# Performance work log

Measured on AMD Instinct MI355X. Metric: run time of the kernel, lower is better.

The kernel has to match this reference:

```python
import jax, jax.numpy as jnp
import numpy as np

B, EMB, ARRAY = 4096, 512, 2
KW = KH = KC = 8
OC = 16                      # output_channel per branch
RED = OC * 2                 # SE hidden width
NUM_REL = 500
FC_IN = 3 * OC * KH * KW * KC  # 24576, flattened concat of 3 branches


def _make_chequer_perm():
    # Deterministic replication of MSLE.get_chequer_perm (perm=1).
    rng = np.random.RandomState(0)
    ent_perm = rng.permutation(EMB * (ARRAY - 1))
    rel_perm = rng.permutation(EMB)
    idxs, ei, ri = [], 0, 0
    for i in range(KC):
        for j in range(KH):
            for k in range(KW):
                for m in range(ARRAY):
                    if (i + j) % ARRAY == m:
                        idxs.append(int(rel_perm[ri]) + EMB * (ARRAY - 1)); ri += 1
                    else:
                        idxs.append(int(ent_perm[ei])); ei += 1
    return jnp.asarray(np.asarray(idxs, dtype=np.int32))


def setup_inputs() -> dict:
    key = jax.random.key(0)
    ks = jax.random.split(key, 12)
    n = lambda k, shape, s=0.05: jax.random.normal(k, shape, jnp.float32) * s
    f1_dim = ARRAY * OC * 1 * 1 * ARRAY        # (1,1,2) kernels
    f3_dim = ARRAY * OC * 1 * ARRAY * ARRAY    # (1,2,2) kernels
    f5_dim = ARRAY * OC * ARRAY * ARRAY * ARRAY  # (2,2,2) kernels
    z = lambda shape: jnp.zeros(shape, jnp.float32)
    o = lambda shape: jnp.ones(shape, jnp.float32)
    return {
        "concat_input": jax.random.normal(ks[0], (B, EMB * ARRAY), jnp.float32),
        "rel": jax.random.randint(ks[1], (B,), 0, NUM_REL),
        "chequer_perm": _make_chequer_perm(),
        "f1_table": n(ks[2], (NUM_REL, f1_dim)),
        "f3_table": n(ks[3], (NUM_REL, f3_dim)),
        "f5_table": n(ks[4], (NUM_REL, f5_dim)),
        "bn0_g": o((ARRAY,)), "bn0_b": z((ARRAY,)),
        "bn1_g": o((OC,)), "bn1_b": z((OC,)),
        "bn2_g": o((OC,)), "bn2_b": z((OC,)),
        "bn3_g": o((OC,)), "bn3_b": z((OC,)),
        "att_Wsq": n(ks[5], (OC, RED)), "att_bsq": z((RED,)),
        "att_W1": n(ks[6], (RED, OC)), "att_b1": z((OC,)),
        "att_W2": n(ks[7], (RED, OC)), "att_b2": z((OC,)),
        "att_W3": n(ks[8], (RED, OC)), "att_b3": z((OC,)),
        "fc_W": n(ks[9], (FC_IN, EMB), 0.01), "fc_b": z((EMB,)),
    }


def _bn(x, g, b, eps=1e-5):
    # BatchNorm3d, training-mode batch statistics over (N, D, H, W).
    m = x.mean(axis=(0, 2, 3, 4), keepdims=True)
    v = x.var(axis=(0, 2, 3, 4), keepdims=True)
    sh = (1, -1, 1, 1, 1)
    return (x - m) * jax.lax.rsqrt(v + eps) * g.reshape(sh) + b.reshape(sh)


def _per_sample_conv(x, w):
    # x: (B, Cin, D, H, W); w: (B, Cout, Cin, kd, kh, kw). 'same' padding,
    # even kernels pad the extra element at the high end (torch padding='same').
    conv1 = lambda xb, wb: jax.lax.conv_general_dilated(
        xb[None], wb, (1, 1, 1), 'SAME',
        dimension_numbers=('NCDHW', 'OIDHW', 'NCDHW'))[0]
    return jax.vmap(conv1)(x, w)


def reference(concat_input, rel, chequer_perm, f1_table, f3_table, f5_table,
              bn0_g, bn0_b, bn1_g, bn1_b, bn2_g, bn2_b, bn3_g, bn3_b,
              att_Wsq, att_bsq, att_W1, att_b1, att_W2, att_b2, att_W3, att_b3,
              fc_W, fc_b):
    b = concat_input.shape[0]
    # Chequered interleave of entity / relation embedding dims.
    x = concat_input[:, chequer_perm].reshape(b, ARRAY, KW, KH, KC)
    x = _bn(x, bn0_g, bn0_b)  # dropout = identity (eval)
    # Per-sample dynamic filters from relation embeddings.
    f1 = f1_table[rel].reshape(b, OC, ARRAY, 1, 1, ARRAY)
    f3 = f3_table[rel].reshape(b, OC, ARRAY, 1, ARRAY, ARRAY)
    f5 = f5_table[rel].reshape(b, OC, ARRAY, ARRAY, ARRAY, ARRAY)
    x1 = _bn(_per_sample_conv(x, f1), bn1_g, bn1_b)
    x3 = _bn(_per_sample_conv(x, f3), bn2_g, bn2_b)
    x5 = _bn(_per_sample_conv(x, f5), bn3_g, bn3_b)
    xs = x1 + x3 + x5
    # SE-style 3D attention: global pool -> shared squeeze -> 3 sigmoid gates.
    pooled = xs.mean(axis=(2, 3, 4))                       # (B, OC)
    zq = jax.nn.relu(pooled @ att_Wsq + att_bsq)           # (B, RED)
    gate = lambda W, bb: jax.nn.sigmoid(zq @ W + bb)[:, :, None, None, None]
    x1 = x1 * gate(att_W1, att_b1)
    x3 = x3 * gate(att_W2, att_b2)
    x5 = x5 * gate(att_W3, att_b3)
    out = jax.nn.relu(jnp.concatenate([x1, x3, x5], axis=1))
    out = out.reshape(b, -1)                               # (B, FC_IN)
    return out @ fc_W + fc_b                               # (B, EMB)
```

## Files before the change

### kernel.cpp

```cpp
#include <hip/hip_runtime.h>
#include <hip/hip_bf16.h>
#include <stdint.h>

typedef short s16x8 __attribute__((ext_vector_type(8)));
typedef short s16x4 __attribute__((ext_vector_type(4)));
typedef float f32x4 __attribute__((ext_vector_type(4)));

#define NB 4096
#define KTOT 24576
#define NOUT 512
#define NCH 48

__device__ __forceinline__ short f2bf(float f){
  union { float f; uint32_t u; } x; x.f = f;
  uint32_t r = (x.u + 0x7FFFu + ((x.u >> 16) & 1u)) >> 16;
  return (short)r;
}
__device__ __forceinline__ float bf2f(short s){
  union { uint32_t u; float f; } x; x.u = ((uint32_t)(uint16_t)s) << 16;
  return x.f;
}
__device__ __forceinline__ short f2bf_fast(float x){
  union { __hip_bfloat16 h; short s; } c; c.h = __float2bfloat16(x); return c.s;
}

#define GLOAD16(g, l) __builtin_amdgcn_global_load_lds( \
  (const __attribute__((address_space(1))) void*)(g), \
  (__attribute__((address_space(3))) void*)(l), 16, 0, 0)

__global__ __launch_bounds__(256) void k_colmap(const int* __restrict__ perm,
                                                int* __restrict__ chmap,
                                                float* __restrict__ statf){
  int q = blockIdx.x * 256 + threadIdx.x;
  if (q < 1024) chmap[perm[q]] = q >> 9;
  if (blockIdx.x == 0 && threadIdx.x < 4) statf[threadIdx.x] = 0.f;
}

__global__ __launch_bounds__(256) void k_bn0(const float* __restrict__ concat,
                                             const int* __restrict__ chmap,
                                             float* __restrict__ statf){
  int t = threadIdx.x;
  float s0=0,q0=0,s1=0,q1=0;
  for (int idx = blockIdx.x*256 + t; idx < NB*1024; idx += gridDim.x*256){
    float v = concat[idx];
    int ch = chmap[idx & 1023];
    if (ch){ s1 += v; q1 += v*v; } else { s0 += v; q0 += v*v; }
  }
  #pragma unroll
  for (int m=1;m<64;m<<=1){
    s0 += __shfl_xor(s0,m); q0 += __shfl_xor(q0,m);
    s1 += __shfl_xor(s1,m); q1 += __shfl_xor(q1,m);
  }
  __shared__ float lb[4][4];
  int wid = t>>6, lane = t&63;
  if (lane==0){ lb[wid][0]=s0; lb[wid][1]=q0; lb[wid][2]=s1; lb[wid][3]=q1; }
  __syncthreads();
  if (t==0){
    float a0=0,a1=0,a2=0,a3=0;
    #pragma unroll
    for (int w=0;w<4;w++){ a0+=lb[w][0]; a1+=lb[w][1]; a2+=lb[w][2]; a3+=lb[w][3]; }
    atomicAdd(&statf[0],a0); atomicAdd(&statf[1],a1);
    atomicAdd(&statf[2],a2); atomicAdd(&statf[3],a3);
  }
}

__global__ __launch_bounds__(256) void k_wcast(const float* __restrict__ fcW,
                                               short* __restrict__ wT){
  __shared__ float tile[64][65];
  int bid = blockIdx.x;
  int kb = (bid % 384) * 64;
  int nb = (bid / 384) * 64;
  int t = threadIdx.x;
  #pragma unroll
  for (int i=0;i<16;i++){
    int r = i*4 + (t>>6), c = t & 63;
    tile[r][c] = fcW[(size_t)(kb + r)*NOUT + nb + c];
  }
  __syncthreads();
  #pragma unroll
  for (int i=0;i<16;i++){
    int n = i*4 + (t>>6), k = t & 63;
    wT[(size_t)(nb + n)*KTOT + kb + k] = f2bf(tile[k][n]);
  }
}

__global__ __launch_bounds__(256) void k_conv(
    const float* __restrict__ concat, const int* __restrict__ perm,
    const int* __restrict__ rel,
    const float* __restrict__ f1t, const float* __restrict__ f3t,
    const float* __restrict__ f5t,
    const float* __restrict__ statf,
    const float* __restrict__ bn0g, const float* __restrict__ bn0b,
    short* __restrict__ raw, float* __restrict__ psum, float* __restrict__ psq)
{
  const int b = blockIdx.x;
  const int t = threadIdx.x;
  __shared__ float xn[2*9*9*9];
  __shared__ float filt[448];
  for (int i=t;i<1458;i+=256) xn[i]=0.f;
  int r = rel[b];
  for (int i=t;i<448;i+=256){
    float v;
    if (i < 64)       v = f1t[r*64 + i];
    else if (i < 192) v = f3t[r*128 + (i-64)];
    else              v = f5t[r*256 + (i-192)];
    filt[i]=v;
  }
  __syncthreads();
  const float n0inv = 1.f/(4096.f*512.f);
  float m0 = statf[0]*n0inv, e0 = statf[1]*n0inv;
  float m1 = statf[2]*n0inv, e1 = statf[3]*n0inv;
  float sc0 = bn0g[0]*rsqrtf(e0-m0*m0+1e-5f), sh0 = bn0b[0]-m0*sc0;
  float sc1 = bn0g[1]*rsqrtf(e1-m1*m1+1e-5f), sh1 = bn0b[1]-m1*sc1;
  for (int q=t;q<1024;q+=256){
    int col = perm[q];
    float v = concat[(size_t)b*1024 + col];
    int ch = q>>9, s = q & 511;
    int d = s>>6, h=(s>>3)&7, w=s&7;
    xn[ch*729 + d*81 + h*9 + w] = ch ? v*sc1+sh1 : v*sc0+sh0;
  }
  __syncthreads();

  const int wid = t>>6, lane = t&63;
  const int d = lane>>3, h = lane&7;
  float r00[9], r01[9], r10[9], r11[9], r20[9], r21[9], r30[9], r31[9];
  #pragma unroll
  for (int w9=0;w9<9;w9++){
    int base0 = d*81 + h*9 + w9;
    int base1 = d*81 + (h+1)*9 + w9;
    int base2 = (d+1)*81 + h*9 + w9;
    int base3 = (d+1)*81 + (h+1)*9 + w9;
    r00[w9]=xn[base0];      r01[w9]=xn[729+base0];
    r10[w9]=xn[base1];      r11[w9]=xn[729+base1];
    r20[w9]=xn[base2];      r21[w9]=xn[729+base2];
    r30[w9]=xn[base3];      r31[w9]=xn[729+base3];
  }
  const size_t rawbase = (size_t)b*KTOT;

  auto finish = [&](int c, const float* v){
    float s=0,q=0;
    #pragma unroll
    for (int p=0;p<8;p++){ s += v[p]; q += v[p]*v[p]; }
    #pragma unroll
    for (int m=1;m<64;m<<=1){ s += __shfl_xor(s,m); q += __shfl_xor(q,m); }
    if (lane==0){ psum[c*NB+b]=s; psq[c*NB+b]=q; }
    s16x8 pk;
    #pragma unroll
    for (int p=0;p<8;p++) pk[p] = f2bf(v[p]);
    *reinterpret_cast<s16x8*>(raw + rawbase + (size_t)c*512 + lane*8) = pk;
  };

  #pragma unroll
  for (int i=0;i<4;i++){
    int oc = wid + 4*i;
    float c0=filt[oc*4+0], c1=filt[oc*4+1], c2=filt[oc*4+2], c3=filt[oc*4+3];
    float v[8];
    #pragma unroll
    for (int p=0;p<8;p++)
      v[p] = c0*r00[p]+c1*r00[p+1]+c2*r01[p]+c3*r01[p+1];
    finish(oc, v);
  }
  #pragma unroll
  for (int i=0;i<4;i++){
    int oc = wid + 4*i;
    const float* cf = &filt[64 + oc*8];
    float v[8];
    #pragma unroll
    for (int p=0;p<8;p++)
      v[p] = cf[0]*r00[p]+cf[1]*r00[p+1]+cf[2]*r10[p]+cf[3]*r10[p+1]
           + cf[4]*r01[p]+cf[5]*r01[p+1]+cf[6]*r11[p]+cf[7]*r11[p+1];
    finish(16+oc, v);
  }
  #pragma unroll
  for (int i=0;i<4;i++){
    int oc = wid + 4*i;
    const float* cf = &filt[192 + oc*16];
    float v[8];
    #pragma unroll
    for (int p=0;p<8;p++)
      v[p] = cf[0]*r00[p] +cf[1]*r00[p+1] +cf[2]*r10[p] +cf[3]*r10[p+1]
           + cf[4]*r20[p] +cf[5]*r20[p+1] +cf[6]*r30[p] +cf[7]*r30[p+1]
           + cf[8]*r01[p] +cf[9]*r01[p+1] +cf[10]*r11[p]+cf[11]*r11[p+1]
           + cf[12]*r21[p]+cf[13]*r21[p+1]+cf[14]*r31[p]+cf[15]*r31[p+1];
    finish(32+oc, v);
  }
}

__global__ __launch_bounds__(256) void k_bnstats(
    const float* __restrict__ psum, const float* __restrict__ psq,
    const float* __restrict__ bn1g, const float* __restrict__ bn1b,
    const float* __restrict__ bn2g, const float* __restrict__ bn2b,
    const float* __restrict__ bn3g, const float* __restrict__ bn3b,
    float* __restrict__ statf)
{
  int c = blockIdx.x, t = threadIdx.x;
  float s=0,q=0;
  for (int b=t;b<NB;b+=256){ s += psum[c*NB+b]; q += psq[c*NB+b]; }
  #pragma unroll
  for (int m=1;m<64;m<<=1){ s += __shfl_xor(s,m); q += __shfl_xor(q,m); }
  __shared__ float lb[4][2];
  int wid = t>>6, lane = t&63;
  if (lane==0){ lb[wid][0]=s; lb[wid][1]=q; }
  __syncthreads();
  if (t==0){
    s = lb[0][0]+lb[1][0]+lb[2][0]+lb[3][0];
    q = lb[0][1]+lb[1][1]+lb[2][1]+lb[3][1];
    float n = 4096.f*512.f;
    float mean = s/n, var = q/n - mean*mean;
    const float* g  = c<16 ? bn1g : (c<32 ? bn2g : bn3g);
    const float* bb = c<16 ? bn1b : (c<32 ? bn2b : bn3b);
    int oc = c & 15;
    float sc = g[oc]*rsqrtf(var + 1e-5f);
    statf[16+c] = sc;
    statf[64+c] = bb[oc] - mean*sc;
  }
}

__global__ __launch_bounds__(64) void k_se(
    const float* __restrict__ psum, const float* __restrict__ statf,
    const float* __restrict__ Wsq, const float* __restrict__ bsq,
    const float* __restrict__ W1, const float* __restrict__ b1,
    const float* __restrict__ W2, const float* __restrict__ b2,
    const float* __restrict__ W3, const float* __restrict__ b3,
    float* __restrict__ gates)
{
  int b = blockIdx.x, lane = threadIdx.x;
  __shared__ float pooled[16];
  __shared__ float zq[32];
  if (lane < 16){
    float p = 0.f;
    #pragma unroll
    for (int br=0;br<3;br++){
      int c = br*16 + lane;
      p += psum[c*NB+b]*(1.f/512.f)*statf[16+c] + statf[64+c];
    }
    pooled[lane] = p;
  }
  __syncthreads();
  if (lane < 32){
    float z = bsq[lane];
    #pragma unroll
    for (int oc=0;oc<16;oc++) z += pooled[oc]*Wsq[oc*32+lane];
    zq[lane] = fmaxf(z, 0.f);
  }
  __syncthreads();
  if (lane < 48){
    int br = lane>>4, oc = lane&15;
    const float* W  = br==0 ? W1 : (br==1 ? W2 : W3);
    const float* bb = br==0 ? b1 : (br==1 ? b2 : b3);
    float g = bb[oc];
    #pragma unroll
    for (int r2=0;r2<32;r2++) g += zq[r2]*W[r2*16+oc];
    gates[lane*NB + b] = 1.f/(1.f + expf(-g));
  }
}

__global__ __launch_bounds__(512, 4) void k_gemm(
    const short* __restrict__ raw, const short* __restrict__ wT,
    const float* __restrict__ scale, const float* __restrict__ shift,
    const float* __restrict__ gates, short* __restrict__ partials)
{
  const int t = threadIdx.x;
  const int bid = blockIdx.x;
  const int sk = bid >> 6, rem = bid & 63;
  const int nblk = rem >> 5, mblk = rem & 31;
  const int b0 = mblk*128, n0 = nblk*256;
  const int kb0 = sk*3072;

  __shared__ short As[2][128][40];
  __shared__ short Ws[2][8192];

  const int wid = t>>6, lane = t&63;

  const int arow = t>>2, acol = (t&3)<<3;
  const short* aptr = raw + (size_t)(b0+arow)*KTOT + kb0 + acol;

  const int nl0 = wid*32 + (lane>>2);
  const int nl1 = nl0 + 16;
  const int sl0 = (lane&3) ^ ((nl0>>1)&3);
  const int sl1 = (lane&3) ^ ((nl1>>1)&3);
  const short* wp0 = wT + (size_t)(n0+nl0)*KTOT + kb0 + sl0*8;
  const short* wp1 = wT + (size_t)(n0+nl1)*KTOT + kb0 + sl1*8;
  const int ldsw0 = wid*1024;
  const int ldsw1 = wid*1024 + 512;

  f32x4 acc[4][4];
  #pragma unroll
  for (int m=0;m<4;m++)
    #pragma unroll
    for (int n=0;n<4;n++){ f32x4 z = {0.f,0.f,0.f,0.f}; acc[m][n]=z; }

  const int wr = (wid>>2)*64, wc = (wid&3)*64;
  const int fr = lane&15, fkq = lane>>4;

  int wroff[4];
  #pragma unroll
  for (int n=0;n<4;n++){
    int r = wc + n*16 + fr;
    wroff[n] = r*64 + ((fkq ^ ((r>>1)&3))<<4);
  }

  GLOAD16(wp0, &Ws[0][ldsw0]);
  GLOAD16(wp1, &Ws[0][ldsw1]);
  s16x8 aReg = *reinterpret_cast<const s16x8*>(aptr);
  int ch = kb0 >> 9;
  float g = gates[ch*NB + b0 + arow];
  float scg = scale[ch]*g, shg = shift[ch]*g;
  {
    s16x8 av;
    #pragma unroll
    for (int j=0;j<8;j++)
      av[j] = f2bf_fast(fmaxf(bf2f(aReg[j])*scg + shg, 0.f));
    *reinterpret_cast<s16x8*>(&As[0][arow][acol]) = av;
  }
  __syncthreads();

  int cur = 0;
  for (int step=0; step<96; ++step){
    const int nxt = cur ^ 1;
    if (step < 95){
      const int ko = (step+1)*32;
      GLOAD16(wp0 + ko, &Ws[nxt][ldsw0]);
      GLOAD16(wp1 + ko, &Ws[nxt][ldsw1]);
      aReg = *reinterpret_cast<const s16x8*>(aptr + ko);
      int nch = (kb0 + ko) >> 9;
      if (nch != ch){
        ch = nch;
        g = gates[ch*NB + b0 + arow];
        scg = scale[ch]*g; shg = shift[ch]*g;
      }
    }
    {
      const short* asb = &As[cur][0][0];
      const char*  wsb = (const char*)&Ws[cur][0];
      s16x8 af[4], bfm[4];
      #pragma unroll
      for (int m=0;m<4;m++)
        af[m] = *reinterpret_cast<const s16x8*>(asb + (wr + m*16 + fr)*40 + fkq*8);
      #pragma unroll
      for (int n=0;n<4;n++)
        bfm[n] = *reinterpret_cast<const s16x8*>(wsb + wroff[n]);
      #pragma unroll
      for (int m=0;m<4;m++)
        #pragma unroll
        for (int n=0;n<4;n++)
          acc[m][n] = __builtin_amdgcn_mfma_f32_16x16x32_bf16(af[m], bfm[n], acc[m][n], 0,0,0);
    }
    if (step < 95){
      s16x8 av;
      #pragma unroll
      for (int j=0;j<8;j++)
        av[j] = f2bf_fast(fmaxf(bf2f(aReg[j])*scg + shg, 0.f));
      *reinterpret_cast<s16x8*>(&As[nxt][arow][acol]) = av;
    }
    __syncthreads();
    cur = nxt;
  }

  short* pb = partials + (size_t)sk*NB*NOUT;
  #pragma unroll
  for (int m=0;m<4;m++){
    #pragma unroll
    for (int j=0;j<4;j++){
      int row = b0 + wr + m*16 + (lane>>4)*4 + j;
      short* prow = pb + (size_t)row*NOUT + n0 + wc + fr;
      #pragma unroll
      for (int n=0;n<4;n++) prow[n*16] = f2bf(acc[m][n][j]);
    }
  }
}

__global__ __launch_bounds__(256) void k_red(const short* __restrict__ partials,
                                             const float* __restrict__ fcb,
                                             float* __restrict__ out){
  int i = blockIdx.x*256 + threadIdx.x;
  int base = i*4;
  f32x4 v = *reinterpret_cast<const f32x4*>(fcb + (base & 511));
  #pragma unroll
  for (int sk=0;sk<8;sk++){
    s16x4 p = *reinterpret_cast<const s16x4*>(partials + (size_t)sk*2097152 + base);
    v[0] += bf2f(p[0]); v[1] += bf2f(p[1]);
    v[2] += bf2f(p[2]); v[3] += bf2f(p[3]);
  }
  *reinterpret_cast<f32x4*>(out + base) = v;
}

extern "C" void kernel_launch(void* const* d_in, const int* in_sizes, int n_in,
                              void* d_out, int out_size, void* d_ws, size_t ws_size,
                              hipStream_t stream) {
  const float* concat = (const float*)d_in[0];
  const int*   rel    = (const int*)  d_in[1];
  const int*   perm   = (const int*)  d_in[2];
  const float* f1t = (const float*)d_in[3];
  const float* f3t = (const float*)d_in[4];
  const float* f5t = (const float*)d_in[5];
  const float* bn0g=(const float*)d_in[6],  *bn0b=(const float*)d_in[7];
  const float* bn1g=(const float*)d_in[8],  *bn1b=(const float*)d_in[9];
  const float* bn2g=(const float*)d_in[10], *bn2b=(const float*)d_in[11];
  const float* bn3g=(const float*)d_in[12], *bn3b=(const float*)d_in[13];
  const float* Wsq=(const float*)d_in[14],  *bsq=(const float*)d_in[15];
  const float* W1=(const float*)d_in[16],   *b1=(const float*)d_in[17];
  const float* W2=(const float*)d_in[18],   *b2=(const float*)d_in[19];
  const float* W3=(const float*)d_in[20],   *b3=(const float*)d_in[21];
  const float* fcW=(const float*)d_in[22],  *fcb=(const float*)d_in[23];
  float* out = (float*)d_out;
  char* ws = (char*)d_ws;

  const size_t off_raw  = 0;
  const size_t off_wT   = 201326592;
  const size_t off_part = 226492416;
  const size_t off_psum = 260046848;
  const size_t off_psq  = 260833280;
  const size_t off_gate = 261619712;
  const size_t off_stat = 262406144;
  const size_t off_chm  = 262406656;
  const size_t need     = off_chm + 4096;
  if (ws_size < need) return;

  short* raw      = (short*)(ws + off_raw);
  short* wT       = (short*)(ws + off_wT);
  short* partials = (short*)(ws + off_part);
  float* psum     = (float*)(ws + off_psum);
  float* psq      = (float*)(ws + off_psq);
  float* gates    = (float*)(ws + off_gate);
  float* statf    = (float*)(ws + off_stat);
  int*   chmap    = (int*)  (ws + off_chm);

  k_colmap<<<4, 256, 0, stream>>>(perm, chmap, statf);
  k_bn0   <<<2048, 256, 0, stream>>>(concat, chmap, statf);
  k_wcast <<<3072, 256, 0, stream>>>(fcW, wT);
  k_conv  <<<4096, 256, 0, stream>>>(concat, perm, rel, f1t, f3t, f5t,
                                     statf, bn0g, bn0b, raw, psum, psq);
  k_bnstats<<<48, 256, 0, stream>>>(psum, psq, bn1g, bn1b, bn2g, bn2b,
                                    bn3g, bn3b, statf);
  k_se    <<<4096, 64, 0, stream>>>(psum, statf, Wsq, bsq, W1, b1, W2, b2,
                                    W3, b3, gates);
  k_gemm  <<<512, 512, 0, stream>>>(raw, wT, statf+16, statf+64, gates, partials);
  k_red   <<<2048, 256, 0, stream>>>(partials, fcb, out);
}
```

Measured before the change: 362.7 us.

## Enlarge GEMM tile to 256x256x64 with XOR-swizzled weights and explicit waitcnt pipelining

The split-K GEMM now uses 256x256 output tiles with a K step of 64, and 8x4 MFMA accumulators per wave, launched as 256 blocks. The weight cast kernel writes fcW pre-swizzled so direct global-to-LDS loads land conflict-free. Per-channel scale/shift times gate values are precomputed into LDS. The main loop uses manual vmcnt/lgkmcnt waits, raw barriers and setprio to overlap loads with MFMA. The aim is more data reuse per tile and fewer barriers, at the cost of higher register and LDS use and only one wave of blocks across the CUs.

```diff
diff --git a/kernel.cpp b/kernel.cpp
--- a/kernel.cpp
+++ b/kernel.cpp
@@ -65,7 +65,7 @@
 }
 
 __global__ __launch_bounds__(256) void k_wcast(const float* __restrict__ fcW,
-                                               short* __restrict__ wT){
+                                               short* __restrict__ wTs){
   __shared__ float tile[64][65];
   int bid = blockIdx.x;
   int kb = (bid % 384) * 64;
@@ -80,7 +80,9 @@
   #pragma unroll
   for (int i=0;i<16;i++){
     int n = i*4 + (t>>6), k = t & 63;
-    wT[(size_t)(nb + n)*KTOT + kb + k] = f2bf(tile[k][n]);
+    int nr = nb + n;
+    int ks = (((k>>3) ^ (nr&7))<<3) | (k&7);
+    wTs[(size_t)nr*KTOT + kb + ks] = f2bf(tile[k][n]);
   }
 }
 
@@ -146,7 +148,7 @@
     if (lane==0){ psum[c*NB+b]=s; psq[c*NB+b]=q; }
     s16x8 pk;
     #pragma unroll
-    for (int p=0;p<8;p++) pk[p] = f2bf(v[p]);
+    for (int p=0;p<8;p++) pk[p] = f2bf_fast(v[p]);
     *reinterpret_cast<s16x8*>(raw + rawbase + (size_t)c*512 + lane*8) = pk;
   };
 
@@ -255,117 +257,166 @@
   }
 }
 
-__global__ __launch_bounds__(512, 4) void k_gemm(
-    const short* __restrict__ raw, const short* __restrict__ wT,
+__global__ __launch_bounds__(512, 2) void k_gemm(
+    const short* __restrict__ raw, const short* __restrict__ wTs,
     const float* __restrict__ scale, const float* __restrict__ shift,
     const float* __restrict__ gates, short* __restrict__ partials)
 {
   const int t = threadIdx.x;
   const int bid = blockIdx.x;
-  const int sk = bid >> 6, rem = bid & 63;
-  const int nblk = rem >> 5, mblk = rem & 31;
-  const int b0 = mblk*128, n0 = nblk*256;
+  const int sk = bid >> 5, rem = bid & 31;
+  const int nblk = rem >> 4, mblk = rem & 15;
+  const int b0 = mblk*256, n0 = nblk*256;
   const int kb0 = sk*3072;
 
-  __shared__ short As[2][128][40];
-  __shared__ short Ws[2][8192];
+  __shared__ short Al[2][256*64];
+  __shared__ short Wl[2][256*64];
+  __shared__ float gsc[6*256];
+  __shared__ float gsh[6*256];
 
   const int wid = t>>6, lane = t&63;
-
-  const int arow = t>>2, acol = (t&3)<<3;
-  const short* aptr = raw + (size_t)(b0+arow)*KTOT + kb0 + acol;
-
-  const int nl0 = wid*32 + (lane>>2);
-  const int nl1 = nl0 + 16;
-  const int sl0 = (lane&3) ^ ((nl0>>1)&3);
-  const int sl1 = (lane&3) ^ ((nl1>>1)&3);
-  const short* wp0 = wT + (size_t)(n0+nl0)*KTOT + kb0 + sl0*8;
-  const short* wp1 = wT + (size_t)(n0+nl1)*KTOT + kb0 + sl1*8;
-  const int ldsw0 = wid*1024;
-  const int ldsw1 = wid*1024 + 512;
-
-  f32x4 acc[4][4];
-  #pragma unroll
-  for (int m=0;m<4;m++)
+  const int wm = wid>>2, wn = wid&3;
+  const int fr = lane&15, fkq = lane>>4;
+  const int sbase = fkq ^ (fr&7);
+
+  for (int i=t; i<1536; i+=512){
+    int c = i>>8, r2 = i&255;
+    int ch = sk*6 + c;
+    float g = gates[(size_t)ch*NB + b0 + r2];
+    gsc[i] = scale[ch]*g;
+    gsh[i] = shift[ch]*g;
+  }
+  __syncthreads();
+
+  const int ar = t>>1, ah = t&1;
+  const short* aptr = raw + (size_t)(b0+ar)*KTOT + kb0 + ah*32;
+  const int arow7 = ar & 7;
+  const short* wbase = wTs + (size_t)(n0 + wid*32)*KTOT + kb0;
+  const int wl_row = lane>>3, wl_g = lane&7;
+
+  f32x4 acc[8][4];
+  #pragma unroll
+  for (int m=0;m<8;m++)
     #pragma unroll
     for (int n=0;n<4;n++){ f32x4 z = {0.f,0.f,0.f,0.f}; acc[m][n]=z; }
 
-  const int wr = (wid>>2)*64, wc = (wid&3)*64;
-  const int fr = lane&15, fkq = lane>>4;
-
-  int wroff[4];
-  #pragma unroll
-  for (int n=0;n<4;n++){
-    int r = wc + n*16 + fr;
-    wroff[n] = r*64 + ((fkq ^ ((r>>1)&3))<<4);
-  }
-
-  GLOAD16(wp0, &Ws[0][ldsw0]);
-  GLOAD16(wp1, &Ws[0][ldsw1]);
-  s16x8 aReg = *reinterpret_cast<const s16x8*>(aptr);
-  int ch = kb0 >> 9;
-  float g = gates[ch*NB + b0 + arow];
-  float scg = scale[ch]*g, shg = shift[ch]*g;
+  s16x8 aR[4];
+
   {
-    s16x8 av;
-    #pragma unroll
-    for (int j=0;j<8;j++)
-      av[j] = f2bf_fast(fmaxf(bf2f(aReg[j])*scg + shg, 0.f));
-    *reinterpret_cast<s16x8*>(&As[0][arow][acol]) = av;
-  }
-  __syncthreads();
+    s16x8 aR0[4];
+    #pragma unroll
+    for (int i=0;i<4;i++) aR0[i] = *reinterpret_cast<const s16x8*>(aptr + i*8);
+    asm volatile("" ::: "memory");
+    #pragma unroll
+    for (int i=0;i<4;i++)
+      GLOAD16(wbase + (size_t)(i*8 + wl_row)*KTOT + wl_g*8, &Wl[0][(wid*32 + i*8)*64]);
+    asm volatile("" ::: "memory");
+    #pragma unroll
+    for (int i=0;i<4;i++) aR[i] = *reinterpret_cast<const s16x8*>(aptr + 64 + i*8);
+    asm volatile("" ::: "memory");
+    #pragma unroll
+    for (int i=0;i<4;i++)
+      GLOAD16(wbase + (size_t)(i*8 + wl_row)*KTOT + 64 + wl_g*8, &Wl[1][(wid*32 + i*8)*64]);
+    asm volatile("s_waitcnt vmcnt(12)" ::: "memory");
+    const float scg = gsc[ar], shg = gsh[ar];
+    #pragma unroll
+    for (int i=0;i<4;i++){
+      s16x8 av;
+      #pragma unroll
+      for (int j=0;j<8;j++)
+        av[j] = f2bf_fast(fmaxf(bf2f(aR0[i][j])*scg + shg, 0.f));
+      int slot = (ah*4 + i) ^ arow7;
+      *reinterpret_cast<s16x8*>(&Al[0][ar*64 + slot*8]) = av;
+    }
+    asm volatile("s_waitcnt lgkmcnt(0)" ::: "memory");
+    __builtin_amdgcn_s_barrier();
+  }
 
   int cur = 0;
-  for (int step=0; step<96; ++step){
-    const int nxt = cur ^ 1;
-    if (step < 95){
-      const int ko = (step+1)*32;
-      GLOAD16(wp0 + ko, &Ws[nxt][ldsw0]);
-      GLOAD16(wp1 + ko, &Ws[nxt][ldsw1]);
-      aReg = *reinterpret_cast<const s16x8*>(aptr + ko);
-      int nch = (kb0 + ko) >> 9;
-      if (nch != ch){
-        ch = nch;
-        g = gates[ch*NB + b0 + arow];
-        scg = scale[ch]*g; shg = shift[ch]*g;
-      }
-    }
-    {
-      const short* asb = &As[cur][0][0];
-      const char*  wsb = (const char*)&Ws[cur][0];
-      s16x8 af[4], bfm[4];
-      #pragma unroll
-      for (int m=0;m<4;m++)
-        af[m] = *reinterpret_cast<const s16x8*>(asb + (wr + m*16 + fr)*40 + fkq*8);
+  for (int it=0; it<47; ++it){
+    asm volatile("s_waitcnt vmcnt(8)" ::: "memory");
+    const short* Ac = &Al[cur][0];
+    const short* Wc = &Wl[cur][0];
+    #pragma unroll
+    for (int ks=0; ks<2; ks++){
+      const int so = ((sbase ^ (ks<<2))<<3);
+      s16x8 af[8], bf[4];
+      #pragma unroll
+      for (int m=0;m<8;m++)
+        af[m] = *reinterpret_cast<const s16x8*>(Ac + (wm*128 + m*16 + fr)*64 + so);
       #pragma unroll
       for (int n=0;n<4;n++)
-        bfm[n] = *reinterpret_cast<const s16x8*>(wsb + wroff[n]);
-      #pragma unroll
-      for (int m=0;m<4;m++)
+        bf[n] = *reinterpret_cast<const s16x8*>(Wc + (wn*64 + n*16 + fr)*64 + so);
+      __builtin_amdgcn_s_setprio(1);
+      #pragma unroll
+      for (int m=0;m<8;m++)
         #pragma unroll
         for (int n=0;n<4;n++)
-          acc[m][n] = __builtin_amdgcn_mfma_f32_16x16x32_bf16(af[m], bfm[n], acc[m][n], 0,0,0);
-    }
-    if (step < 95){
-      s16x8 av;
-      #pragma unroll
-      for (int j=0;j<8;j++)
-        av[j] = f2bf_fast(fmaxf(bf2f(aReg[j])*scg + shg, 0.f));
-      *reinterpret_cast<s16x8*>(&As[nxt][arow][acol]) = av;
-    }
-    __syncthreads();
-    cur = nxt;
+          acc[m][n] = __builtin_amdgcn_mfma_f32_16x16x32_bf16(af[m], bf[n], acc[m][n], 0,0,0);
+      __builtin_amdgcn_s_setprio(0);
+    }
+    asm volatile("s_waitcnt vmcnt(4)" ::: "memory");
+    {
+      const int c = (it+1)>>3;
+      const float scg = gsc[c*256 + ar], shg = gsh[c*256 + ar];
+      short* An = &Al[cur^1][0];
+      #pragma unroll
+      for (int i=0;i<4;i++){
+        s16x8 av;
+        #pragma unroll
+        for (int j=0;j<8;j++)
+          av[j] = f2bf_fast(fmaxf(bf2f(aR[i][j])*scg + shg, 0.f));
+        int slot = (ah*4 + i) ^ arow7;
+        *reinterpret_cast<s16x8*>(An + ar*64 + slot*8) = av;
+      }
+    }
+    asm volatile("s_waitcnt lgkmcnt(0)" ::: "memory");
+    __builtin_amdgcn_s_barrier();
+    if (it < 46){
+      const int ko = (it+2)*64;
+      #pragma unroll
+      for (int i=0;i<4;i++) aR[i] = *reinterpret_cast<const s16x8*>(aptr + ko + i*8);
+      asm volatile("" ::: "memory");
+      #pragma unroll
+      for (int i=0;i<4;i++)
+        GLOAD16(wbase + (size_t)(i*8 + wl_row)*KTOT + ko + wl_g*8, &Wl[cur][(wid*32 + i*8)*64]);
+      asm volatile("" ::: "memory");
+    }
+    cur ^= 1;
+  }
+  asm volatile("s_waitcnt vmcnt(0)" ::: "memory");
+  {
+    const short* Ac = &Al[cur][0];
+    const short* Wc = &Wl[cur][0];
+    #pragma unroll
+    for (int ks=0; ks<2; ks++){
+      const int so = ((sbase ^ (ks<<2))<<3);
+      s16x8 af[8], bf[4];
+      #pragma unroll
+      for (int m=0;m<8;m++)
+        af[m] = *reinterpret_cast<const s16x8*>(Ac + (wm*128 + m*16 + fr)*64 + so);
+      #pragma unroll
+      for (int n=0;n<4;n++)
+        bf[n] = *reinterpret_cast<const s16x8*>(Wc + (wn*64 + n*16 + fr)*64 + so);
+      __builtin_amdgcn_s_setprio(1);
+      #pragma unroll
+      for (int m=0;m<8;m++)
+        #pragma unroll
+        for (int n=0;n<4;n++)
+          acc[m][n] = __builtin_amdgcn_mfma_f32_16x16x32_bf16(af[m], bf[n], acc[m][n], 0,0,0);
+      __builtin_amdgcn_s_setprio(0);
+    }
   }
 
   short* pb = partials + (size_t)sk*NB*NOUT;
   #pragma unroll
-  for (int m=0;m<4;m++){
+  for (int m=0;m<8;m++){
     #pragma unroll
     for (int j=0;j<4;j++){
-      int row = b0 + wr + m*16 + (lane>>4)*4 + j;
-      short* prow = pb + (size_t)row*NOUT + n0 + wc + fr;
-      #pragma unroll
-      for (int n=0;n<4;n++) prow[n*16] = f2bf(acc[m][n][j]);
+      int row = b0 + wm*128 + m*16 + fkq*4 + j;
+      short* prow = pb + (size_t)row*NOUT + n0 + wn*64 + fr;
+      #pragma unroll
+      for (int n=0;n<4;n++) prow[n*16] = f2bf_fast(acc[m][n][j]);
     }
   }
 }
@@ -418,7 +469,7 @@
   if (ws_size < need) return;
 
   short* raw      = (short*)(ws + off_raw);
-  short* wT       = (short*)(ws + off_wT);
+  short* wTs      = (short*)(ws + off_wT);
   short* partials = (short*)(ws + off_part);
   float* psum     = (float*)(ws + off_psum);
   float* psq      = (float*)(ws + off_psq);
@@ -428,13 +479,13 @@
 
   k_colmap<<<4, 256, 0, stream>>>(perm, chmap, statf);
   k_bn0   <<<2048, 256, 0, stream>>>(concat, chmap, statf);
-  k_wcast <<<3072, 256, 0, stream>>>(fcW, wT);
+  k_wcast <<<3072, 256, 0, stream>>>(fcW, wTs);
   k_conv  <<<4096, 256, 0, stream>>>(concat, perm, rel, f1t, f3t, f5t,
                                      statf, bn0g, bn0b, raw, psum, psq);
   k_bnstats<<<48, 256, 0, stream>>>(psum, psq, bn1g, bn1b, bn2g, bn2b,
                                     bn3g, bn3b, statf);
   k_se    <<<4096, 64, 0, stream>>>(psum, statf, Wsq, bsq, W1, b1, W2, b2,
                                     W3, b3, gates);
-  k_gemm  <<<512, 512, 0, stream>>>(raw, wT, statf+16, statf+64, gates, partials);
+  k_gemm  <<<256, 512, 0, stream>>>(raw, wTs, statf+16, statf+64, gates, partials);
   k_red   <<<2048, 256, 0, stream>>>(partials, fcb, out);
 }
```

After: 358.1 us. About the same (-1.3%).
